# Performance work log

Hardware: AMD Instinct MI355X
Metric: run time of the kernel (lower is better)

Reference implementation:

```python
import jax, jax.numpy as jnp
import numpy as np

N_VARS = 524288      # number of input variables
WIDTH = 524288       # output width of every layer (csr[-1]+1)
FANIN = 8            # children per output node -> unrolled csr = repeat(arange(WIDTH), FANIN)
N_LAYERS = 8         # alternating SumLayer (even, log-prod) / LogSumLayer (odd, log-sum)
N_EDGES = WIDTH * FANIN
EPS = 1e-15          # epsilon used by _logsumexp_scatter_reduce (torch.full init + scatter_add)
CUTOFF = -float(np.log(2.0))


def log1mexp(x):
    # numerically accurate log(1 - exp(x)) for x < 0 (eps=0 as in forward default)
    return jnp.where(x > CUTOFF, jnp.log(-jnp.expm1(x)), jnp.log1p(-jnp.exp(x)))


def setup_inputs() -> dict:
    key = jax.random.key(0)
    ks = jax.random.split(key, 1 + N_LAYERS)
    # weights are log-probabilities: log(u), u in (0.01, 0.99)
    u = jax.random.uniform(ks[0], (N_VARS,), minval=0.01, maxval=0.99, dtype=jnp.float32)
    weights = jnp.log(u)
    in0 = 2 + 2 * N_VARS  # size of encode_input output
    ptr_list = [jax.random.randint(ks[1], (N_EDGES,), 0, in0, dtype=jnp.int32)]
    for i in range(1, N_LAYERS):
        ptr_list.append(jax.random.randint(ks[1 + i], (N_EDGES,), 0, WIDTH, dtype=jnp.int32))
    ptrs = jnp.stack(ptr_list)                                   # [L, E]
    csr = jnp.repeat(jnp.arange(WIDTH, dtype=jnp.int32), FANIN)  # unrolled CSR segment ids
    csrs = jnp.broadcast_to(csr, (N_LAYERS, N_EDGES))            # [L, E]
    return {"weights": weights, "ptrs": ptrs, "csrs": csrs}


def _forward(weights, ptrs, csrs):
    # encode_input: [zero, one, w0, neg_w0, w1, neg_w1, ...]; log semiring: zero=-inf, one=0
    neg = log1mexp(weights)
    consts = jnp.array([-jnp.inf, 0.0], dtype=weights.dtype)
    x = jnp.concatenate([consts, jnp.stack([weights, neg], axis=1).ravel()])
    for i in range(N_LAYERS):
        g = x[ptrs[i]]            # gather: x[self.ptrs]
        seg = csrs[i]
        if i % 2 == 0:
            # SumLayer: scatter_reduce 'sum' over CSR segments (log-space product)
            x = jax.ops.segment_sum(g, seg, num_segments=WIDTH)
        else:
            # LogSumLayer: stabilized scatter-logsumexp
            m = jax.lax.stop_gradient(jax.ops.segment_max(g, seg, num_segments=WIDTH))
            y = jnp.nan_to_num(g - m[seg], nan=0.0, posinf=jnp.inf, neginf=-jnp.inf)
            s = jax.ops.segment_sum(jnp.exp(y), seg, num_segments=WIDTH) + EPS
            x = jnp.log(s) + m
    return x


def reference(weights, ptrs, csrs):
    return _forward(weights, ptrs, csrs)
```

## Files before the change

### kernel.cpp

```cpp
#include <hip/hip_runtime.h>
#include <math.h>

#define NVARS   524288
#define WIDTH   524288
#define FANIN   8
#define NEDGES  (WIDTH * FANIN)
#define ENC_PAD 1048592

#define TPB     256
#define NBLK    (WIDTH / TPB)

typedef int v4i __attribute__((ext_vector_type(4)));

__device__ __forceinline__ v4i nt_load4(const int* p) {
    return __builtin_nontemporal_load((const v4i*)p);
}

__device__ __forceinline__ float encode_neg(float wi) {
    return (wi > -0.69314718055994530942f) ? logf(-expm1f(wi))
                                           : log1pf(-expf(wi));
}

__device__ __forceinline__ void gather8_sc0(const float* __restrict__ x,
                                            v4i a, v4i b,
                                            float& g0, float& g1, float& g2, float& g3,
                                            float& g4, float& g5, float& g6, float& g7) {
    const float* p0 = x + a.x;  const float* p1 = x + a.y;
    const float* p2 = x + a.z;  const float* p3 = x + a.w;
    const float* p4 = x + b.x;  const float* p5 = x + b.y;
    const float* p6 = x + b.z;  const float* p7 = x + b.w;
    asm volatile(
        "global_load_dword %0, %8,  off sc0\n\t"
        "global_load_dword %1, %9,  off sc0\n\t"
        "global_load_dword %2, %10, off sc0\n\t"
        "global_load_dword %3, %11, off sc0\n\t"
        "global_load_dword %4, %12, off sc0\n\t"
        "global_load_dword %5, %13, off sc0\n\t"
        "global_load_dword %6, %14, off sc0\n\t"
        "global_load_dword %7, %15, off sc0\n\t"
        "s_waitcnt vmcnt(0)"
        : "=&v"(g0), "=&v"(g1), "=&v"(g2), "=&v"(g3),
          "=&v"(g4), "=&v"(g5), "=&v"(g6), "=&v"(g7)
        : "v"(p0), "v"(p1), "v"(p2), "v"(p3),
          "v"(p4), "v"(p5), "v"(p6), "v"(p7));
}

__global__ __launch_bounds__(256) void encode_kernel(const float* __restrict__ w,
                                                     float* __restrict__ x) {
    int i = blockIdx.x * blockDim.x + threadIdx.x;
    if (i == 0) { x[0] = -__builtin_inff(); x[1] = 0.0f; }
    if (i < NVARS) {
        float wi = w[i];
        x[2 + 2 * i] = wi;
        x[3 + 2 * i] = encode_neg(wi);
    }
}

template <int IS_LSE>
__global__ __launch_bounds__(256) void layer_kernel(const int* __restrict__ ptr,
                                                    const float* __restrict__ x,
                                                    float* __restrict__ y) {
    const int i = blockIdx.x * blockDim.x + threadIdx.x;

    v4i a = nt_load4(ptr + 8 * (size_t)i);
    v4i b = nt_load4(ptr + 8 * (size_t)i + 4);

    float g0, g1, g2, g3, g4, g5, g6, g7;
    gather8_sc0(x, a, b, g0, g1, g2, g3, g4, g5, g6, g7);

    float r;
    if (IS_LSE) {
        float m = fmaxf(fmaxf(fmaxf(g0, g1), fmaxf(g2, g3)),
                        fmaxf(fmaxf(g4, g5), fmaxf(g6, g7)));
        float s = (__expf(g0 - m) + __expf(g1 - m))
                + (__expf(g2 - m) + __expf(g3 - m))
                + (__expf(g4 - m) + __expf(g5 - m))
                + (__expf(g6 - m) + __expf(g7 - m)) + 1e-15f;
        float lse = __logf(s) + m;
        r = (m == -__builtin_inff()) ? -__builtin_inff() : lse;
    } else {
        r = ((g0 + g1) + (g2 + g3)) + ((g4 + g5) + (g6 + g7));
    }

    y[i] = r;
}

extern "C" void kernel_launch(void* const* d_in, const int* in_sizes, int n_in,
                              void* d_out, int out_size, void* d_ws, size_t ws_size,
                              hipStream_t stream) {
    const float* w    = (const float*)d_in[0];
    const int*   ptrs = (const int*)d_in[1];
    float* out = (float*)d_out;
    float* ws  = (float*)d_ws;

    float* enc  = ws;
    float* bufA = ws + ENC_PAD;
    float* bufB = bufA + WIDTH;

    encode_kernel<<<NVARS / 256, 256, 0, stream>>>(w, enc);

    layer_kernel<0><<<NBLK, TPB, 0, stream>>>(ptrs + (size_t)0 * NEDGES, enc,  bufA);
    layer_kernel<1><<<NBLK, TPB, 0, stream>>>(ptrs + (size_t)1 * NEDGES, bufA, bufB);
    layer_kernel<0><<<NBLK, TPB, 0, stream>>>(ptrs + (size_t)2 * NEDGES, bufB, bufA);
    layer_kernel<1><<<NBLK, TPB, 0, stream>>>(ptrs + (size_t)3 * NEDGES, bufA, bufB);
    layer_kernel<0><<<NBLK, TPB, 0, stream>>>(ptrs + (size_t)4 * NEDGES, bufB, bufA);
    layer_kernel<1><<<NBLK, TPB, 0, stream>>>(ptrs + (size_t)5 * NEDGES, bufA, bufB);
    layer_kernel<0><<<NBLK, TPB, 0, stream>>>(ptrs + (size_t)6 * NEDGES, bufB, bufA);
    layer_kernel<1><<<NBLK, TPB, 0, stream>>>(ptrs + (size_t)7 * NEDGES, bufA, out);
}
```

Baseline: 184.8 us.

## Fuse input encoding into first layer gather and drop inline-asm gathers

Removes the separate encode kernel and computes encoded input values on the fly inside the first layer, gathering directly from the weight array. The encoded buffer write/read and one launch go away, but each gathered edge now recomputes exp/log, and the accurate log1mexp branch is replaced by a fast __logf(1-__expf) form that may lose precision near zero. The other layers switch from inline-asm sc0 loads to plain C++ indexed loads, which lets the compiler schedule them but drops the cache hint.

```diff
diff --git a/kernel.cpp b/kernel.cpp
--- a/kernel.cpp
+++ b/kernel.cpp
@@ -16,44 +16,29 @@
     return __builtin_nontemporal_load((const v4i*)p);
 }
 
-__device__ __forceinline__ float encode_neg(float wi) {
-    return (wi > -0.69314718055994530942f) ? logf(-expm1f(wi))
-                                           : log1pf(-expf(wi));
+__device__ __forceinline__ float enc_at(const float* __restrict__ w, int j) {
+    int k = (j - 2) >> 1;
+    k = k < 0 ? 0 : k;
+    float v = w[k];
+    float neg = __logf(1.0f - __expf(v));
+    float r = (j & 1) ? neg : v;
+    if (j < 2) r = (j == 0) ? -__builtin_inff() : 0.0f;
+    return r;
 }
 
-__device__ __forceinline__ void gather8_sc0(const float* __restrict__ x,
-                                            v4i a, v4i b,
-                                            float& g0, float& g1, float& g2, float& g3,
-                                            float& g4, float& g5, float& g6, float& g7) {
-    const float* p0 = x + a.x;  const float* p1 = x + a.y;
-    const float* p2 = x + a.z;  const float* p3 = x + a.w;
-    const float* p4 = x + b.x;  const float* p5 = x + b.y;
-    const float* p6 = x + b.z;  const float* p7 = x + b.w;
-    asm volatile(
-        "global_load_dword %0, %8,  off sc0\n\t"
-        "global_load_dword %1, %9,  off sc0\n\t"
-        "global_load_dword %2, %10, off sc0\n\t"
-        "global_load_dword %3, %11, off sc0\n\t"
-        "global_load_dword %4, %12, off sc0\n\t"
-        "global_load_dword %5, %13, off sc0\n\t"
-        "global_load_dword %6, %14, off sc0\n\t"
-        "global_load_dword %7, %15, off sc0\n\t"
-        "s_waitcnt vmcnt(0)"
-        : "=&v"(g0), "=&v"(g1), "=&v"(g2), "=&v"(g3),
-          "=&v"(g4), "=&v"(g5), "=&v"(g6), "=&v"(g7)
-        : "v"(p0), "v"(p1), "v"(p2), "v"(p3),
-          "v"(p4), "v"(p5), "v"(p6), "v"(p7));
-}
+__global__ __launch_bounds__(256) void layer0_kernel(const int* __restrict__ ptr,
+                                                     const float* __restrict__ w,
+                                                     float* __restrict__ y) {
+    const int i = blockIdx.x * blockDim.x + threadIdx.x;
+    v4i a = nt_load4(ptr + 8 * (size_t)i);
+    v4i b = nt_load4(ptr + 8 * (size_t)i + 4);
 
-__global__ __launch_bounds__(256) void encode_kernel(const float* __restrict__ w,
-                                                     float* __restrict__ x) {
-    int i = blockIdx.x * blockDim.x + threadIdx.x;
-    if (i == 0) { x[0] = -__builtin_inff(); x[1] = 0.0f; }
-    if (i < NVARS) {
-        float wi = w[i];
-        x[2 + 2 * i] = wi;
-        x[3 + 2 * i] = encode_neg(wi);
-    }
+    float g0 = enc_at(w, a.x), g1 = enc_at(w, a.y);
+    float g2 = enc_at(w, a.z), g3 = enc_at(w, a.w);
+    float g4 = enc_at(w, b.x), g5 = enc_at(w, b.y);
+    float g6 = enc_at(w, b.z), g7 = enc_at(w, b.w);
+
+    y[i] = ((g0 + g1) + (g2 + g3)) + ((g4 + g5) + (g6 + g7));
 }
 
 template <int IS_LSE>
@@ -65,8 +50,8 @@
     v4i a = nt_load4(ptr + 8 * (size_t)i);
     v4i b = nt_load4(ptr + 8 * (size_t)i + 4);
 
-    float g0, g1, g2, g3, g4, g5, g6, g7;
-    gather8_sc0(x, a, b, g0, g1, g2, g3, g4, g5, g6, g7);
+    float g0 = x[a.x], g1 = x[a.y], g2 = x[a.z], g3 = x[a.w];
+    float g4 = x[b.x], g5 = x[b.y], g6 = x[b.z], g7 = x[b.w];
 
     float r;
     if (IS_LSE) {
@@ -93,13 +78,11 @@
     float* out = (float*)d_out;
     float* ws  = (float*)d_ws;
 
-    float* enc  = ws;
-    float* bufA = ws + ENC_PAD;
+    float* bufA = ws;
     float* bufB = bufA + WIDTH;
 
-    encode_kernel<<<NVARS / 256, 256, 0, stream>>>(w, enc);
+    layer0_kernel<<<NBLK, TPB, 0, stream>>>(ptrs + (size_t)0 * NEDGES, w, bufA);
 
-    layer_kernel<0><<<NBLK, TPB, 0, stream>>>(ptrs + (size_t)0 * NEDGES, enc,  bufA);
     layer_kernel<1><<<NBLK, TPB, 0, stream>>>(ptrs + (size_t)1 * NEDGES, bufA, bufB);
     layer_kernel<0><<<NBLK, TPB, 0, stream>>>(ptrs + (size_t)2 * NEDGES, bufB, bufA);
     layer_kernel<1><<<NBLK, TPB, 0, stream>>>(ptrs + (size_t)3 * NEDGES, bufA, bufB);
```

Measured after the change: 177.9 us. 1.04x faster.
